# Kernel optimization log

Hardware: AMD Instinct MI355X
Metric: run time of the kernel (lower is better)

## Reference

```python
import jax, jax.numpy as jnp
import numpy as np
import math

EMBED_DIM = 1024
NUM_HEADS = 16
HEAD_DIM = EMBED_DIM // NUM_HEADS
BLOCK_SIZE = 64
NUM_RAND_BLOCKS = 3
B, L = 2, 2048


def _build_sparse_mask(seq_len, block_size, num_rand_blocks, seed=0):
    """BigBird block-sparse mask: global (first/last block) + window (prev/self/next) + random blocks."""
    nb = seq_len // block_size
    bm = np.zeros((nb, nb), dtype=bool)
    # global: first and last blocks attend to all / are attended by all
    bm[0, :] = True
    bm[:, 0] = True
    bm[-1, :] = True
    bm[:, -1] = True
    # sliding window for interior blocks
    for b in range(1, nb - 1):
        bm[b, max(b - 1, 0):b + 2] = True
    # random blocks for interior blocks (deterministic for reproducibility)
    rng = np.random.default_rng(seed)
    for b in range(1, nb - 1):
        avail = [x for x in range(nb) if x != b]
        picks = rng.permutation(len(avail))[:num_rand_blocks]
        for p in picks:
            bm[b, avail[p]] = True
    # expand block mask to token-level [L, L]
    return np.kron(bm, np.ones((block_size, block_size), dtype=bool))


def setup_inputs() -> dict:
    key = jax.random.key(0)
    k0, k1, k2, k3, k4 = jax.random.split(key, 5)
    hidden_states = jax.random.normal(k0, (B, L, EMBED_DIM), dtype=jnp.float32)
    s = 0.02
    # torch nn.Linear weights have shape [out_features, in_features]
    Wq = jax.random.normal(k1, (EMBED_DIM, EMBED_DIM), dtype=jnp.float32) * s
    Wk = jax.random.normal(k2, (EMBED_DIM, EMBED_DIM), dtype=jnp.float32) * s
    Wv = jax.random.normal(k3, (EMBED_DIM, EMBED_DIM), dtype=jnp.float32) * s
    Wo = jax.random.normal(k4, (EMBED_DIM, EMBED_DIM), dtype=jnp.float32) * s
    sparse_mask = jnp.asarray(_build_sparse_mask(L, BLOCK_SIZE, NUM_RAND_BLOCKS))
    return {"hidden_states": hidden_states, "Wq": Wq, "Wk": Wk, "Wv": Wv,
            "Wo": Wo, "sparse_mask": sparse_mask}


def reference(hidden_states, Wq, Wk, Wv, Wo, sparse_mask):
    Bsz, Lq, D = hidden_states.shape
    H, hd = NUM_HEADS, HEAD_DIM
    # projections (Linear no bias): x @ W.T
    q = (hidden_states @ Wq.T).reshape(Bsz, Lq, H, hd).transpose(0, 2, 1, 3)
    k = (hidden_states @ Wk.T).reshape(Bsz, Lq, H, hd).transpose(0, 2, 1, 3)
    v = (hidden_states @ Wv.T).reshape(Bsz, Lq, H, hd).transpose(0, 2, 1, 3)
    # dense scores with block-sparse mask (matches reference module's math)
    scores = jnp.einsum('bhqd,bhkd->bhqk', q, k) / math.sqrt(hd)  # [B,H,L,L]
    scores = jnp.where(sparse_mask[None, None, :, :], scores, -jnp.inf)
    attn = jax.nn.softmax(scores.astype(jnp.float32), axis=-1).astype(scores.dtype)
    out = jnp.einsum('bhqk,bhkd->bhqd', attn, v)
    out = out.transpose(0, 2, 1, 3).reshape(Bsz, Lq, D)
    out = out @ Wo.T
    return out
```

## Files before the change

kernel.cpp:

```cpp
#include <hip/hip_runtime.h>
#include <hip/hip_bf16.h>
#include <stdint.h>

#define LSEQ   2048
#define DMODEL 1024
#define NHEADS 16
#define HDIM   64
#define NB     32
#define BATCH  2
#define NGRP   38
#define NWG_ATTN (32 * NGRP)

typedef unsigned short u16;
typedef __attribute__((ext_vector_type(8))) __bf16 bf16x8;
typedef __attribute__((ext_vector_type(4))) float f32x4;
typedef __attribute__((ext_vector_type(4))) unsigned int u32x4;
typedef __attribute__((ext_vector_type(4))) u16 u16x4;


__device__ __forceinline__ u16 f2b(float f) {
  unsigned b = __float_as_uint(f);
  return (u16)((b + 0x7FFFu + ((b >> 16) & 1u)) >> 16);
}

__device__ __forceinline__ void lds_dma16(const u16* g, u16* l) {
  __builtin_amdgcn_global_load_lds(
      (__attribute__((address_space(1))) const void*)g,
      (__attribute__((address_space(3))) void*)l, 16, 0, 0);
}

__device__ __forceinline__ bool probe_is_bf16(const void* src) {
  const u16* p = (const u16*)src;
  int cnt = 0;
  #pragma unroll
  for (int i = 0; i < 64; ++i) {
    int e = (p[i] >> 7) & 0xFF;
    cnt += (e >= 100 && e <= 140) ? 1 : 0;
  }
  return cnt >= 48;
}

__device__ __forceinline__ bool mask_block(const void* m, int qb, int kb) {
  const unsigned char* p = (const unsigned char*)m;
  size_t e = (size_t)(qb * 64) * LSEQ + (size_t)kb * 64;
  unsigned char b0 = p[0], b1 = p[1], b2 = p[2];
  if (b0 == 1 && b1 == 1) return p[e] != 0;
  if (b0 == 1 && b1 == 0 && b2 == 1) return ((const u16*)m)[e] != 0;
  if (b0 == 1) return ((const unsigned int*)m)[e] != 0;
  if (b0 == 0x80 && b1 == 0x3f) return ((const u16*)m)[e] != 0;
  return ((const float*)m)[e] != 0.0f;
}

__global__ __launch_bounds__(256) void convert_kernel(
    const void* __restrict__ hs, const void* __restrict__ wq,
    const void* __restrict__ wk, const void* __restrict__ wv,
    const void* __restrict__ wo, u16* __restrict__ dst,
    const void* __restrict__ mask, int* __restrict__ skb,
    f32x4* __restrict__ zbuf, int zn4) {
  __shared__ int sflag;
  if (threadIdx.x == 0) sflag = probe_is_bf16(hs) ? 1 : 0;
  __syncthreads();
  bool isbf = sflag != 0;
  if (blockIdx.x == 0 && threadIdx.x < NB) {
    int qb = threadIdx.x;
    int base = (qb == 0) ? 0 : ((qb == 31) ? 32 : (64 + (qb - 1) * 8));
    int cap = (qb == 0 || qb == 31) ? 32 : 8;
    int c = 0;
    for (int kb = 0; kb < NB; ++kb)
      if (mask_block(mask, qb, kb)) skb[base + c++] = kb;
    for (; c < cap; ++c) skb[base + c] = -1;
  }
  const int HS4 = BATCH * LSEQ * DMODEL / 4;
  const int W4 = DMODEL * DMODEL / 4;
  int total4 = HS4 + 4 * W4;
  int stride = gridDim.x * blockDim.x;
  for (int i = blockIdx.x * blockDim.x + threadIdx.x; i < total4; i += stride) {
    const void* src;
    int off;
    if (i < HS4) { src = hs; off = i; }
    else {
      int j = i - HS4;
      int wsel = j >> 18;
      off = j & (W4 - 1);
      src = (wsel == 0) ? wq : (wsel == 1) ? wk : (wsel == 2) ? wv : wo;
    }
    u16x4 v;
    if (isbf) v = ((const u16x4*)src)[off];
    else {
      f32x4 f = ((const f32x4*)src)[off];
      v = (u16x4){f2b(f[0]), f2b(f[1]), f2b(f[2]), f2b(f[3])};
    }
    ((u16x4*)dst)[i] = v;
  }
  for (int i = blockIdx.x * blockDim.x + threadIdx.x; i < zn4; i += stride)
    zbuf[i] = (f32x4){0.f, 0.f, 0.f, 0.f};
}

#define GBK 32
#define TN  128

template <int TM>
__global__ __launch_bounds__(256) void gemm_bt(
    const u16* __restrict__ A, const u16* __restrict__ Bw,
    void* __restrict__ C, u16* __restrict__ C2, int M, int N, int K,
    int layout, int is_final, const void* __restrict__ probe_src) {
  constexpr int NJ = (TM == 128) ? 4 : 2;
  __shared__ u16 lA[TM * 32];
  __shared__ int sflag;
  int t = threadIdx.x;
  int w = t >> 6, l = t & 63, q4 = l >> 4, lc = l & 15;
  int lr = l >> 2, lcc = l & 3;
  int tileM = blockIdx.x * TM, tileN = blockIdx.y * TN;
  int wm = (TM == 128) ? (w >> 1) * 64 : 0;
  int wn = (TM == 128) ? (w & 1) * 64 : w * 32;
  if (t == 0) sflag = (is_final && !probe_is_bf16(probe_src)) ? 0 : 1;

  f32x4 acc[4][NJ] = {};

  for (int kt = 0; kt < K; kt += GBK) {
    bf16x8 bf[NJ];
    #pragma unroll
    for (int j = 0; j < NJ; ++j)
      bf[j] = *(const bf16x8*)(Bw + (size_t)(tileN + wn + j * 16 + lc) * K + kt + q4 * 8);

    __syncthreads();
    #pragma unroll
    for (int it = 0; it < TM / 64; ++it) {
      int m = w * (TM / 64) + it;
      int row = m * 16 + lr;
      lds_dma16(A + (size_t)(tileM + row) * K + kt + lcc * 8, lA + m * 512);
    }
    __syncthreads();

    bf16x8 af[4];
    #pragma unroll
    for (int i = 0; i < 4; ++i)
      af[i] = *(const bf16x8*)(lA + (wm + i * 16 + lc) * 32 + q4 * 8);
    #pragma unroll
    for (int i = 0; i < 4; ++i)
      #pragma unroll
      for (int j = 0; j < NJ; ++j)
        acc[i][j] = __builtin_amdgcn_mfma_f32_16x16x32_bf16(af[i], bf[j], acc[i][j], 0, 0, 0);
  }

  bool out_bf = sflag != 0;
  #pragma unroll
  for (int i = 0; i < 4; ++i)
    #pragma unroll
    for (int j = 0; j < NJ; ++j) {
      int rowb = tileM + wm + i * 16 + q4 * 4;
      int col = tileN + wn + j * 16 + lc;
      if (layout == 0) {
        #pragma unroll
        for (int r = 0; r < 4; ++r) {
          float v = acc[i][j][r];
          size_t idx = (size_t)(rowb + r) * N + col;
          if (out_bf) ((u16*)C)[idx] = f2b(v);
          else ((float*)C)[idx] = v;
        }
      } else {
        int sel = col >> 10;
        int o = col & 1023;
        int h = o >> 6, d = o & 63;
        int b = rowb >> 11, ll = rowb & 2047;
        if (sel == 2) {
          u16x4 pk = {f2b(acc[i][j][0]), f2b(acc[i][j][1]),
                      f2b(acc[i][j][2]), f2b(acc[i][j][3])};
          *(u16x4*)(C2 + ((size_t)((b * NHEADS + h) * HDIM + d)) * LSEQ + ll) = pk;
        } else {
          float sc = (sel == 0) ? 0.125f : 1.0f;
          #pragma unroll
          for (int r = 0; r < 4; ++r) {
            size_t idx = (size_t)sel * (size_t)(BATCH * NHEADS * LSEQ * HDIM) +
                         (((size_t)(b * NHEADS + h) * LSEQ) + ll + r) * HDIM + d;
            ((u16*)C)[idx] = f2b(acc[i][j][r] * sc);
          }
        }
      }
    }
}

#define LDP 72

__global__ __launch_bounds__(256) void attn_kernel(
    const u16* __restrict__ qb_, const u16* __restrict__ kb_,
    const u16* __restrict__ vt_, const int* __restrict__ skb,
    float* __restrict__ obuf2, float* __restrict__ lbuf2,
    u16* __restrict__ ctx) {
  __shared__ u16 lK[64 * 64];
  __shared__ u16 lV[64 * 64];
  __shared__ u16 lP[4][16 * LDP];
  int i = blockIdx.x;
  int bh = (i & 7) + ((i >> 3) & 3) * 8;
  int g = i >> 5;
  int qb = (g < 4) ? 0 : ((g < 8) ? 31 : (g - 7));
  int t = threadIdx.x, w = t >> 6, l = t & 63, q4 = l >> 4, lc = l & 15;
  int c0 = t, c1 = 256 + t;
  int r0 = c0 >> 3, cc0 = c0 & 7, r1 = c1 >> 3, cc1 = c1 & 7;

  const u16* qp = qb_ + ((size_t)bh * LSEQ + qb * 64 + w * 16 + lc) * HDIM;
  bf16x8 bq0 = *(const bf16x8*)(qp + q4 * 8);
  bf16x8 bq1 = *(const bf16x8*)(qp + 32 + q4 * 8);

  const u16* kp = kb_ + (size_t)bh * LSEQ * HDIM;
  const u16* vp = vt_ + (size_t)bh * HDIM * LSEQ;
  u16* myP = &lP[w][0];

  f32x4 oacc[4];
  #pragma unroll
  for (int d = 0; d < 4; ++d) oacc[d] = (f32x4){0.f, 0.f, 0.f, 0.f};
  float lp = 0.0f;

  for (int it = 0; it < 8; ++it) {
    int kb = skb[g * 8 + it];
    if (kb < 0) break;
    const u16* kblk = kp + (size_t)kb * 64 * HDIM;
    const u16* vblk = vp + kb * 64;
    __syncthreads();
    lds_dma16(kblk + r0 * HDIM + cc0 * 8, lK + w * 512);
    lds_dma16(kblk + r1 * HDIM + cc1 * 8, lK + 2048 + w * 512);
    lds_dma16(vblk + (size_t)r0 * LSEQ + cc0 * 8, lV + w * 512);
    lds_dma16(vblk + (size_t)r1 * LSEQ + cc1 * 8, lV + 2048 + w * 512);
    __syncthreads();

    f32x4 st[4];
    #pragma unroll
    for (int mt = 0; mt < 4; ++mt) {
      bf16x8 k0 = *(const bf16x8*)(lK + (mt * 16 + lc) * 64 + q4 * 8);
      bf16x8 k1 = *(const bf16x8*)(lK + (mt * 16 + lc) * 64 + 32 + q4 * 8);
      f32x4 z = (f32x4){0.f, 0.f, 0.f, 0.f};
      z = __builtin_amdgcn_mfma_f32_16x16x32_bf16(k0, bq0, z, 0, 0, 0);
      z = __builtin_amdgcn_mfma_f32_16x16x32_bf16(k1, bq1, z, 0, 0, 0);
      st[mt] = z;
    }

    #pragma unroll
    for (int mt = 0; mt < 4; ++mt) {
      float p0 = __expf(st[mt][0]), p1 = __expf(st[mt][1]);
      float p2 = __expf(st[mt][2]), p3 = __expf(st[mt][3]);
      lp += (p0 + p1) + (p2 + p3);
      u16x4 pk = {f2b(p0), f2b(p1), f2b(p2), f2b(p3)};
      *(u16x4*)(myP + lc * LDP + mt * 16 + q4 * 4) = pk;
    }

    bf16x8 ap0 = *(const bf16x8*)(myP + lc * LDP + q4 * 8);
    bf16x8 ap1 = *(const bf16x8*)(myP + lc * LDP + 32 + q4 * 8);
    #pragma unroll
    for (int dt = 0; dt < 4; ++dt) {
      bf16x8 v0 = *(const bf16x8*)(lV + (dt * 16 + lc) * 64 + q4 * 8);
      bf16x8 v1 = *(const bf16x8*)(lV + (dt * 16 + lc) * 64 + 32 + q4 * 8);
      oacc[dt] = __builtin_amdgcn_mfma_f32_16x16x32_bf16(ap0, v0, oacc[dt], 0, 0, 0);
      oacc[dt] = __builtin_amdgcn_mfma_f32_16x16x32_bf16(ap1, v1, oacc[dt], 0, 0, 0);
    }
  }

  float ltot = lp;
  ltot += __shfl_xor(ltot, 16);
  ltot += __shfl_xor(ltot, 32);

  if (g >= 8) {
    float inv[4];
    #pragma unroll
    for (int r = 0; r < 4; ++r)
      inv[r] = 1.0f / __shfl(ltot, q4 * 4 + r);
    int b = bh >> 4, h = bh & 15;
    #pragma unroll
    for (int dt = 0; dt < 4; ++dt)
      #pragma unroll
      for (int r = 0; r < 4; ++r) {
        float v = oacc[dt][r] * inv[r];
        int grow = qb * 64 + w * 16 + q4 * 4 + r;
        size_t odx = ((size_t)b * LSEQ + grow) * DMODEL + h * HDIM + dt * 16 + lc;
        ctx[odx] = f2b(v);
      }
  } else {
    int s = (qb == 31) ? 1 : 0;
    if (q4 == 0)
      unsafeAtomicAdd(lbuf2 + ((size_t)bh * 2 + s) * 64 + w * 16 + lc, ltot);
    #pragma unroll
    for (int dt = 0; dt < 4; ++dt)
      #pragma unroll
      for (int r = 0; r < 4; ++r)
        unsafeAtomicAdd(obuf2 + (((size_t)bh * 2 + s) * 64 + w * 16 + q4 * 4 + r) * 64 +
                            dt * 16 + lc, oacc[dt][r]);
  }
}

__global__ __launch_bounds__(256) void normalize2_kernel(
    const float* __restrict__ obuf2, const float* __restrict__ lbuf2,
    u16* __restrict__ ctx) {
  int e4 = blockIdx.x * 256 + threadIdx.x;
  int e = e4 * 4;
  int bh = e >> 13;
  int rem = e & 8191;
  int s = rem >> 12, row = (rem >> 6) & 63, d = rem & 63;
  f32x4 o = *(const f32x4*)(obuf2 + e);
  float linv = 1.0f / lbuf2[(bh * 2 + s) * 64 + row];
  int qb = s ? 31 : 0;
  int b = bh >> 4, h = bh & 15;
  int grow = qb * 64 + row;
  u16x4 pk = {f2b(o[0] * linv), f2b(o[1] * linv), f2b(o[2] * linv), f2b(o[3] * linv)};
  *(u16x4*)(ctx + ((size_t)b * LSEQ + grow) * DMODEL + h * HDIM + d) = pk;
}

extern "C" void kernel_launch(void* const* d_in, const int* in_sizes, int n_in,
                              void* d_out, int out_size, void* d_ws, size_t ws_size,
                              hipStream_t stream) {
  const void* hs = d_in[0];
  const void* wq = d_in[1];
  const void* wk = d_in[2];
  const void* wv = d_in[3];
  const void* wo = d_in[4];
  const void* mask = d_in[5];

  u16* hsb = (u16*)d_ws;
  u16* wqb = hsb + 4 * 1024 * 1024;
  u16* wob = wqb + 3 * 1024 * 1024;
  u16* qbuf = wob + 1024 * 1024;
  u16* kbuf = qbuf + 4 * 1024 * 1024;
  u16* vtb  = kbuf + 4 * 1024 * 1024;
  u16* ctx  = vtb + 4 * 1024 * 1024;
  int* skb  = (int*)(ctx + 4 * 1024 * 1024);
  float* obuf2 = (float*)(skb + 512);
  float* lbuf2 = obuf2 + 32 * 2 * 64 * 64;
  const int ZN4 = (32 * 2 * 64 * 64 + 4096) / 4;

  convert_kernel<<<4096, 256, 0, stream>>>(hs, wq, wk, wv, wo, hsb, mask, skb,
                                           (f32x4*)obuf2, ZN4);

  dim3 gqkv(32, 24);
  gemm_bt<128><<<gqkv, 256, 0, stream>>>(hsb, wqb, qbuf, vtb, 4096, 3072, 1024, 1, 0, hs);

  attn_kernel<<<NWG_ATTN, 256, 0, stream>>>(qbuf, kbuf, vtb, skb, obuf2, lbuf2, ctx);

  normalize2_kernel<<<256, 256, 0, stream>>>(obuf2, lbuf2, ctx);

  dim3 gout(64, 8);
  gemm_bt<64><<<gout, 256, 0, stream>>>(ctx, wob, d_out, nullptr, 4096, 1024, 1024, 0, 1, hs);
}
```

Measured before the change: 231.7 us.

## Skip bf16 conversion pass, stage GEMM B tiles in LDS, batch two KV blocks

The convert kernel now exits early when inputs are already bf16, and the GEMMs read the raw bf16 inputs directly by picking per-tile base pointers. With fp32 inputs they fall back to the converted copies. The GEMM's B operand is now staged into LDS by DMA alongside A instead of being loaded straight from global memory into registers. The attention kernel loads two K/V blocks per barrier phase into doubled LDS buffers, which halves the number of synchronisations at the cost of more LDS per workgroup. With the default fp32 inputs the conversion still runs, so mainly the LDS staging and KV batching take effect.

```diff
diff --git a/kernel.cpp b/kernel.cpp
--- a/kernel.cpp
+++ b/kernel.cpp
@@ -57,10 +57,6 @@
     const void* __restrict__ wo, u16* __restrict__ dst,
     const void* __restrict__ mask, int* __restrict__ skb,
     f32x4* __restrict__ zbuf, int zn4) {
-  __shared__ int sflag;
-  if (threadIdx.x == 0) sflag = probe_is_bf16(hs) ? 1 : 0;
-  __syncthreads();
-  bool isbf = sflag != 0;
   if (blockIdx.x == 0 && threadIdx.x < NB) {
     int qb = threadIdx.x;
     int base = (qb == 0) ? 0 : ((qb == 31) ? 32 : (64 + (qb - 1) * 8));
@@ -70,10 +66,15 @@
       if (mask_block(mask, qb, kb)) skb[base + c++] = kb;
     for (; c < cap; ++c) skb[base + c] = -1;
   }
+  int stride = gridDim.x * blockDim.x;
+  for (int i = blockIdx.x * blockDim.x + threadIdx.x; i < zn4; i += stride)
+    zbuf[i] = (f32x4){0.f, 0.f, 0.f, 0.f};
+
+  if (probe_is_bf16(hs)) return;
+
   const int HS4 = BATCH * LSEQ * DMODEL / 4;
   const int W4 = DMODEL * DMODEL / 4;
   int total4 = HS4 + 4 * W4;
-  int stride = gridDim.x * blockDim.x;
   for (int i = blockIdx.x * blockDim.x + threadIdx.x; i < total4; i += stride) {
     const void* src;
     int off;
@@ -84,16 +85,9 @@
       off = j & (W4 - 1);
       src = (wsel == 0) ? wq : (wsel == 1) ? wk : (wsel == 2) ? wv : wo;
     }
-    u16x4 v;
-    if (isbf) v = ((const u16x4*)src)[off];
-    else {
-      f32x4 f = ((const f32x4*)src)[off];
-      v = (u16x4){f2b(f[0]), f2b(f[1]), f2b(f[2]), f2b(f[3])};
-    }
-    ((u16x4*)dst)[i] = v;
-  }
-  for (int i = blockIdx.x * blockDim.x + threadIdx.x; i < zn4; i += stride)
-    zbuf[i] = (f32x4){0.f, 0.f, 0.f, 0.f};
+    f32x4 f = ((const f32x4*)src)[off];
+    ((u16x4*)dst)[i] = (u16x4){f2b(f[0]), f2b(f[1]), f2b(f[2]), f2b(f[3])};
+  }
 }
 
 #define GBK 32
@@ -101,49 +95,64 @@
 
 template <int TM>
 __global__ __launch_bounds__(256) void gemm_bt(
-    const u16* __restrict__ A, const u16* __restrict__ Bw,
-    void* __restrict__ C, u16* __restrict__ C2, int M, int N, int K,
-    int layout, int is_final, const void* __restrict__ probe_src) {
+    const void* __restrict__ probe_src,
+    const u16* __restrict__ A_bf, const u16* __restrict__ A_alt,
+    const u16* __restrict__ Braw0, const u16* __restrict__ Braw1,
+    const u16* __restrict__ Braw2, const u16* __restrict__ Bconv,
+    void* __restrict__ C, u16* __restrict__ C2, int N, int K, int layout) {
   constexpr int NJ = (TM == 128) ? 4 : 2;
   __shared__ u16 lA[TM * 32];
-  __shared__ int sflag;
+  __shared__ u16 lB[TN * 32];
   int t = threadIdx.x;
   int w = t >> 6, l = t & 63, q4 = l >> 4, lc = l & 15;
   int lr = l >> 2, lcc = l & 3;
   int tileM = blockIdx.x * TM, tileN = blockIdx.y * TN;
   int wm = (TM == 128) ? (w >> 1) * 64 : 0;
   int wn = (TM == 128) ? (w & 1) * 64 : w * 32;
-  if (t == 0) sflag = (is_final && !probe_is_bf16(probe_src)) ? 0 : 1;
+
+  bool bf = probe_is_bf16(probe_src);
+  const u16* A = bf ? A_bf : A_alt;
+  const u16* Bbase;
+  int bOff;
+  if (bf) {
+    Bbase = (tileN < 1024) ? Braw0 : (tileN < 2048) ? Braw1 : Braw2;
+    bOff = tileN & 1023;
+  } else {
+    Bbase = Bconv;
+    bOff = tileN;
+  }
 
   f32x4 acc[4][NJ] = {};
 
   for (int kt = 0; kt < K; kt += GBK) {
-    bf16x8 bf[NJ];
-    #pragma unroll
-    for (int j = 0; j < NJ; ++j)
-      bf[j] = *(const bf16x8*)(Bw + (size_t)(tileN + wn + j * 16 + lc) * K + kt + q4 * 8);
-
     __syncthreads();
     #pragma unroll
     for (int it = 0; it < TM / 64; ++it) {
       int m = w * (TM / 64) + it;
-      int row = m * 16 + lr;
-      lds_dma16(A + (size_t)(tileM + row) * K + kt + lcc * 8, lA + m * 512);
+      lds_dma16(A + (size_t)(tileM + m * 16 + lr) * K + kt + lcc * 8, lA + m * 512);
+    }
+    #pragma unroll
+    for (int it = 0; it < 2; ++it) {
+      int m = w * 2 + it;
+      lds_dma16(Bbase + (size_t)(bOff + m * 16 + lr) * K + kt + lcc * 8, lB + m * 512);
     }
     __syncthreads();
 
-    bf16x8 af[4];
+    bf16x8 af[4], bfr[NJ];
     #pragma unroll
     for (int i = 0; i < 4; ++i)
       af[i] = *(const bf16x8*)(lA + (wm + i * 16 + lc) * 32 + q4 * 8);
     #pragma unroll
+    for (int j = 0; j < NJ; ++j)
+      bfr[j] = *(const bf16x8*)(lB + (wn + j * 16 + lc) * 32 + q4 * 8);
+    #pragma unroll
     for (int i = 0; i < 4; ++i)
       #pragma unroll
       for (int j = 0; j < NJ; ++j)
-        acc[i][j] = __builtin_amdgcn_mfma_f32_16x16x32_bf16(af[i], bf[j], acc[i][j], 0, 0, 0);
-  }
-
-  bool out_bf = sflag != 0;
+        acc[i][j] = __builtin_amdgcn_mfma_f32_16x16x32_bf16(af[i], bfr[j], acc[i][j], 0, 0, 0);
+  }
+
+  bool out_bf = (layout == 1) ? true : bf;
   #pragma unroll
   for (int i = 0; i < 4; ++i)
     #pragma unroll
@@ -187,8 +196,8 @@
     const u16* __restrict__ vt_, const int* __restrict__ skb,
     float* __restrict__ obuf2, float* __restrict__ lbuf2,
     u16* __restrict__ ctx) {
-  __shared__ u16 lK[64 * 64];
-  __shared__ u16 lV[64 * 64];
+  __shared__ u16 lK[2][64 * 64];
+  __shared__ u16 lV[2][64 * 64];
   __shared__ u16 lP[4][16 * LDP];
   int i = blockIdx.x;
   int bh = (i & 7) + ((i >> 3) & 3) * 8;
@@ -211,46 +220,57 @@
   for (int d = 0; d < 4; ++d) oacc[d] = (f32x4){0.f, 0.f, 0.f, 0.f};
   float lp = 0.0f;
 
-  for (int it = 0; it < 8; ++it) {
-    int kb = skb[g * 8 + it];
-    if (kb < 0) break;
-    const u16* kblk = kp + (size_t)kb * 64 * HDIM;
-    const u16* vblk = vp + kb * 64;
+  for (int ph = 0; ph < 4; ++ph) {
+    int kb0 = skb[g * 8 + 2 * ph];
+    if (kb0 < 0) break;
+    int kb1 = skb[g * 8 + 2 * ph + 1];
+    int kb1e = (kb1 < 0) ? kb0 : kb1;
+
     __syncthreads();
-    lds_dma16(kblk + r0 * HDIM + cc0 * 8, lK + w * 512);
-    lds_dma16(kblk + r1 * HDIM + cc1 * 8, lK + 2048 + w * 512);
-    lds_dma16(vblk + (size_t)r0 * LSEQ + cc0 * 8, lV + w * 512);
-    lds_dma16(vblk + (size_t)r1 * LSEQ + cc1 * 8, lV + 2048 + w * 512);
+    #pragma unroll
+    for (int u = 0; u < 2; ++u) {
+      int kbu = u ? kb1e : kb0;
+      const u16* kblk = kp + (size_t)kbu * 64 * HDIM;
+      const u16* vblk = vp + kbu * 64;
+      lds_dma16(kblk + r0 * HDIM + cc0 * 8, lK[u] + w * 512);
+      lds_dma16(kblk + r1 * HDIM + cc1 * 8, lK[u] + 2048 + w * 512);
+      lds_dma16(vblk + (size_t)r0 * LSEQ + cc0 * 8, lV[u] + w * 512);
+      lds_dma16(vblk + (size_t)r1 * LSEQ + cc1 * 8, lV[u] + 2048 + w * 512);
+    }
     __syncthreads();
 
-    f32x4 st[4];
-    #pragma unroll
-    for (int mt = 0; mt < 4; ++mt) {
-      bf16x8 k0 = *(const bf16x8*)(lK + (mt * 16 + lc) * 64 + q4 * 8);
-      bf16x8 k1 = *(const bf16x8*)(lK + (mt * 16 + lc) * 64 + 32 + q4 * 8);
-      f32x4 z = (f32x4){0.f, 0.f, 0.f, 0.f};
-      z = __builtin_amdgcn_mfma_f32_16x16x32_bf16(k0, bq0, z, 0, 0, 0);
-      z = __builtin_amdgcn_mfma_f32_16x16x32_bf16(k1, bq1, z, 0, 0, 0);
-      st[mt] = z;
-    }
-
-    #pragma unroll
-    for (int mt = 0; mt < 4; ++mt) {
-      float p0 = __expf(st[mt][0]), p1 = __expf(st[mt][1]);
-      float p2 = __expf(st[mt][2]), p3 = __expf(st[mt][3]);
-      lp += (p0 + p1) + (p2 + p3);
-      u16x4 pk = {f2b(p0), f2b(p1), f2b(p2), f2b(p3)};
-      *(u16x4*)(myP + lc * LDP + mt * 16 + q4 * 4) = pk;
-    }
-
-    bf16x8 ap0 = *(const bf16x8*)(myP + lc * LDP + q4 * 8);
-    bf16x8 ap1 = *(const bf16x8*)(myP + lc * LDP + 32 + q4 * 8);
-    #pragma unroll
-    for (int dt = 0; dt < 4; ++dt) {
-      bf16x8 v0 = *(const bf16x8*)(lV + (dt * 16 + lc) * 64 + q4 * 8);
-      bf16x8 v1 = *(const bf16x8*)(lV + (dt * 16 + lc) * 64 + 32 + q4 * 8);
-      oacc[dt] = __builtin_amdgcn_mfma_f32_16x16x32_bf16(ap0, v0, oacc[dt], 0, 0, 0);
-      oacc[dt] = __builtin_amdgcn_mfma_f32_16x16x32_bf16(ap1, v1, oacc[dt], 0, 0, 0);
+    #pragma unroll
+    for (int u = 0; u < 2; ++u) {
+      if (u == 1 && kb1 < 0) break;
+      f32x4 st[4];
+      #pragma unroll
+      for (int mt = 0; mt < 4; ++mt) {
+        bf16x8 k0 = *(const bf16x8*)(lK[u] + (mt * 16 + lc) * 64 + q4 * 8);
+        bf16x8 k1 = *(const bf16x8*)(lK[u] + (mt * 16 + lc) * 64 + 32 + q4 * 8);
+        f32x4 z = (f32x4){0.f, 0.f, 0.f, 0.f};
+        z = __builtin_amdgcn_mfma_f32_16x16x32_bf16(k0, bq0, z, 0, 0, 0);
+        z = __builtin_amdgcn_mfma_f32_16x16x32_bf16(k1, bq1, z, 0, 0, 0);
+        st[mt] = z;
+      }
+
+      #pragma unroll
+      for (int mt = 0; mt < 4; ++mt) {
+        float p0 = __expf(st[mt][0]), p1 = __expf(st[mt][1]);
+        float p2 = __expf(st[mt][2]), p3 = __expf(st[mt][3]);
+        lp += (p0 + p1) + (p2 + p3);
+        u16x4 pk = {f2b(p0), f2b(p1), f2b(p2), f2b(p3)};
+        *(u16x4*)(myP + lc * LDP + mt * 16 + q4 * 4) = pk;
+      }
+
+      bf16x8 ap0 = *(const bf16x8*)(myP + lc * LDP + q4 * 8);
+      bf16x8 ap1 = *(const bf16x8*)(myP + lc * LDP + 32 + q4 * 8);
+      #pragma unroll
+      for (int dt = 0; dt < 4; ++dt) {
+        bf16x8 v0 = *(const bf16x8*)(lV[u] + (dt * 16 + lc) * 64 + q4 * 8);
+        bf16x8 v1 = *(const bf16x8*)(lV[u] + (dt * 16 + lc) * 64 + 32 + q4 * 8);
+        oacc[dt] = __builtin_amdgcn_mfma_f32_16x16x32_bf16(ap0, v0, oacc[dt], 0, 0, 0);
+        oacc[dt] = __builtin_amdgcn_mfma_f32_16x16x32_bf16(ap1, v1, oacc[dt], 0, 0, 0);
+      }
     }
   }
 
@@ -307,10 +327,10 @@
                               void* d_out, int out_size, void* d_ws, size_t ws_size,
                               hipStream_t stream) {
   const void* hs = d_in[0];
-  const void* wq = d_in[1];
-  const void* wk = d_in[2];
-  const void* wv = d_in[3];
-  const void* wo = d_in[4];
+  const u16* wq = (const u16*)d_in[1];
+  const u16* wk = (const u16*)d_in[2];
+  const u16* wv = (const u16*)d_in[3];
+  const u16* wo = (const u16*)d_in[4];
   const void* mask = d_in[5];
 
   u16* hsb = (u16*)d_ws;
@@ -329,12 +349,16 @@
                                            (f32x4*)obuf2, ZN4);
 
   dim3 gqkv(32, 24);
-  gemm_bt<128><<<gqkv, 256, 0, stream>>>(hsb, wqb, qbuf, vtb, 4096, 3072, 1024, 1, 0, hs);
+  gemm_bt<128><<<gqkv, 256, 0, stream>>>(hs, (const u16*)hs, hsb,
+                                         wq, wk, wv, wqb,
+                                         qbuf, vtb, 3072, 1024, 1);
 
   attn_kernel<<<NWG_ATTN, 256, 0, stream>>>(qbuf, kbuf, vtb, skb, obuf2, lbuf2, ctx);
 
   normalize2_kernel<<<256, 256, 0, stream>>>(obuf2, lbuf2, ctx);
 
   dim3 gout(64, 8);
-  gemm_bt<64><<<gout, 256, 0, stream>>>(ctx, wob, d_out, nullptr, 4096, 1024, 1024, 0, 1, hs);
-}
+  gemm_bt<64><<<gout, 256, 0, stream>>>(hs, ctx, ctx,
+                                        wo, wo, wo, wob,
+                                        d_out, nullptr, 1024, 1024, 0);
+}
```

New measurement: 213.5 us. 1.08x faster.
